# Kernel tuning notes

Hardware: AMD Instinct MI355X
Metric: run time of the kernel (lower is better)

## Reference

```python
import jax, jax.numpy as jnp
import numpy as np
from itertools import product

NUM_LEVELS = 4
NUM_FEATURES = 4
B, L = 32, 512

def build_kernel(num_features, num_levels):
    # signatory.all_words ordering: words grouped by length 1..num_levels, lexicographic within length
    words = [w for m in range(1, num_levels + 1) for w in product(range(num_features), repeat=m)]
    num_components = num_levels * (num_levels + 1) // 2
    k = np.zeros((num_components, num_features, len(words)), dtype=np.float32)
    for i, word in enumerate(words):
        m = len(word)
        start = m * (m - 1) // 2
        for j, axis in enumerate(word):
            k[start + j, axis, i] = 1.0
    return jnp.asarray(k)

def setup_inputs() -> dict:
    key = jax.random.key(0)
    x = jax.random.normal(key, (B, L, NUM_FEATURES), dtype=jnp.float32)
    return {"x": x, "kernel": build_kernel(NUM_FEATURES, NUM_LEVELS)}

def reference(x, kernel):
    Bn, Ln, F = x.shape
    NF = kernel.shape[-1]  # num_functionals = 340
    # path increments
    seq = x[:, 1:, :] - x[:, :-1, :]                      # (B, L-1, F)
    # lift: (C, B, L-1, NF), C = num_levels*(num_levels+1)/2 = 10
    M = jnp.einsum('blf,cfk->cblk', seq, kernel)
    # level-by-level recursion with independent weights, return_sequences=True
    # then summed over the stacked level axis (stack+sum == running sum of Y terms)
    sig = jnp.cumsum(M[0], axis=1)                        # level 1
    k = 1
    for m in range(1, NUM_LEVELS):
        R = M[k]; k += 1
        for _ in range(m):
            # tf.cumsum(..., exclusive=True) == inclusive cumsum minus self
            R = M[k] * (jnp.cumsum(R, axis=1) - R)
            k += 1
        sig = sig + jnp.cumsum(R, axis=1)
    # prepend zero time step -> (B, L, NF)
    sig = jnp.concatenate([jnp.zeros((Bn, 1, NF), dtype=x.dtype), sig], axis=1)
    # prepend constant-1 functional channel -> (B, L, NF+1)
    return jnp.concatenate([jnp.ones((Bn, Ln, 1), dtype=x.dtype), sig], axis=-1)
```

## Files before the change

### kernel.cpp

```cpp
#include <hip/hip_runtime.h>


#define SIG_B 32
#define SIG_L 512
#define SIG_NSTEP 511
#define SIG_ROW 341
#define SIG_CS 32
#define SIG_C 16
#define SIG_PAD 344

__global__ __launch_bounds__(256) void sigA(const float* __restrict__ x,
                                            float* __restrict__ Lsig) {
    const int bc = blockIdx.x;
    const int b = bc / SIG_C, c = bc % SIG_C;
    const int tid = threadIdx.x;
    const int t0 = c * SIG_CS;
    const int nt = min(SIG_CS, SIG_NSTEP - t0);

    __shared__ float dlds[SIG_CS * 4];
    const float* xb = x + ((size_t)b * SIG_L + t0) * 4;
    if (tid < nt) {
        float4 x0 = *(const float4*)(xb + tid * 4);
        float4 x1 = *(const float4*)(xb + (tid + 1) * 4);
        *(float4*)(dlds + tid * 4) =
            make_float4(x1.x - x0.x, x1.y - x0.y, x1.z - x0.z, x1.w - x0.w);
    }
    __syncthreads();

    const int a = tid >> 6, bb = (tid >> 4) & 3, cc = (tid >> 2) & 3, ee = tid & 3;
    float s1 = 0.f, s2 = 0.f, s3 = 0.f, s4 = 0.f;
    const float* dp = dlds;
    for (int t = 0; t < nt; ++t) {
        const float da = dp[a], db = dp[bb], dc = dp[cc], de = dp[ee];
        dp += 4;
        s4 = fmaf(s3, de, s4);
        s3 = fmaf(s2, dc, s3);
        s2 = fmaf(s1, db, s2);
        s1 += da;
    }
    float* Lr = Lsig + (size_t)bc * SIG_PAD;
    if ((tid & 63) == 0) Lr[1 + a] = s1;
    if ((tid & 15) == 0) Lr[5 + (tid >> 4)] = s2;
    if ((tid & 3) == 0)  Lr[21 + (tid >> 2)] = s3;
    Lr[85 + tid] = s4;
}

__global__ __launch_bounds__(256) void sigC(const float* __restrict__ x,
                                            const float* __restrict__ Lsig,
                                            float* __restrict__ out) {
    const int bc = blockIdx.x;
    const int b = bc / SIG_C, c = bc % SIG_C;
    const int tid = threadIdx.x;
    const int t0 = c * SIG_CS;
    const int nt = min(SIG_CS, SIG_NSTEP - t0);

    __shared__ float dlds[SIG_CS * 4];
    __shared__ float L[SIG_C * SIG_PAD];

    const float* xb = x + ((size_t)b * SIG_L + t0) * 4;
    if (tid < nt) {
        float4 x0 = *(const float4*)(xb + tid * 4);
        float4 x1 = *(const float4*)(xb + (tid + 1) * 4);
        *(float4*)(dlds + tid * 4) =
            make_float4(x1.x - x0.x, x1.y - x0.y, x1.z - x0.z, x1.w - x0.w);
    }
    {
        const float4* Lb4 = (const float4*)(Lsig + (size_t)b * SIG_C * SIG_PAD);
        float4* L4 = (float4*)L;
        const int n4 = c * (SIG_PAD / 4);
        for (int i = tid; i < n4; i += 256) L4[i] = Lb4[i];
    }
    __syncthreads();

    const int a = tid >> 6, bb = (tid >> 4) & 3, cc = (tid >> 2) & 3, ee = tid & 3;

    float p1 = 0.f, p2 = 0.f, p3 = 0.f, p4 = 0.f;
    for (int j = 0; j < c; ++j) {
        const float* Lc = L + j * SIG_PAD;
        const float l1a = Lc[1 + a], l1b = Lc[1 + bb], l1c = Lc[1 + cc], l1e = Lc[1 + ee];
        const float l2ab = Lc[5 + 4 * a + bb], l2bc = Lc[5 + 4 * bb + cc],
                    l2ce = Lc[5 + 4 * cc + ee];
        const float l3abc = Lc[21 + 16 * a + 4 * bb + cc],
                    l3bce = Lc[21 + 16 * bb + 4 * cc + ee];
        const float l4 = Lc[85 + tid];
        p4 += p3 * l1e + p2 * l2ce + p1 * l3bce + l4;
        p3 += p2 * l1c + p1 * l2bc + l3abc;
        p2 += p1 * l1b + l2ab;
        p1 += l1a;
    }

    float s1 = 0.f, s2 = 0.f, s3 = 0.f, s4 = 0.f;
    float x1_ = 0.f, x2_ = 0.f, x3_ = 0.f;
    float v1 = 0.f, v2 = 0.f;
    float u1 = 0.f;

    float* row = out + ((size_t)b * SIG_L + (t0 + 1)) * SIG_ROW;

    if (c == 0) {
        float* r0 = out + (size_t)b * SIG_L * SIG_ROW;
        if (tid == 0)        __builtin_nontemporal_store(1.0f, r0 + 0);
        if ((tid & 63) == 0) __builtin_nontemporal_store(0.f, r0 + 1 + a);
        if ((tid & 15) == 0) __builtin_nontemporal_store(0.f, r0 + 5 + (tid >> 4));
        if ((tid & 3) == 0)  __builtin_nontemporal_store(0.f, r0 + 21 + (tid >> 2));
        __builtin_nontemporal_store(0.f, r0 + 85 + tid);
    }

    const float* dp = dlds;
    for (int t = 0; t < nt; ++t) {
        const float da = dp[a], db = dp[bb], dc = dp[cc], de = dp[ee];
        dp += 4;
        s4 = fmaf(s3, de, s4); s3 = fmaf(s2, dc, s3); s2 = fmaf(s1, db, s2); s1 += da;
        x3_ = fmaf(x2_, de, x3_); x2_ = fmaf(x1_, dc, x2_); x1_ += db;
        v2 = fmaf(v1, de, v2); v1 += dc;
        u1 += de;

        if (tid == 0)        __builtin_nontemporal_store(1.0f, row + 0);
        if ((tid & 63) == 0) __builtin_nontemporal_store(p1 + s1, row + 1 + a);
        if ((tid & 15) == 0) __builtin_nontemporal_store(p2 + p1 * x1_ + s2,
                                                         row + 5 + (tid >> 4));
        if ((tid & 3) == 0)  __builtin_nontemporal_store(p3 + p2 * v1 + p1 * x2_ + s3,
                                                         row + 21 + (tid >> 2));
        __builtin_nontemporal_store(p4 + p3 * u1 + p2 * v2 + p1 * x3_ + s4,
                                    row + 85 + tid);
        row += SIG_ROW;
    }
}

extern "C" void kernel_launch(void* const* d_in, const int* in_sizes, int n_in,
                              void* d_out, int out_size, void* d_ws, size_t ws_size,
                              hipStream_t stream) {
    const float* x = (const float*)d_in[0];
    float* out = (float*)d_out;
    float* Lsig = (float*)d_ws;

    sigA<<<SIG_B * SIG_C, 256, 0, stream>>>(x, Lsig);
    sigC<<<SIG_B * SIG_C, 256, 0, stream>>>(x, Lsig, out);
}
```

Baseline: 22.20 us.

## Halve chunk length, double chunk count, and fully unroll time loops

```diff
diff --git a/kernel.cpp b/kernel.cpp
--- a/kernel.cpp
+++ b/kernel.cpp
@@ -5,8 +5,8 @@
 #define SIG_L 512
 #define SIG_NSTEP 511
 #define SIG_ROW 341
-#define SIG_CS 32
-#define SIG_C 16
+#define SIG_CS 16
+#define SIG_C 32
 #define SIG_PAD 344
 
 __global__ __launch_bounds__(256) void sigA(const float* __restrict__ x,
@@ -19,20 +19,24 @@
 
     __shared__ float dlds[SIG_CS * 4];
     const float* xb = x + ((size_t)b * SIG_L + t0) * 4;
-    if (tid < nt) {
-        float4 x0 = *(const float4*)(xb + tid * 4);
-        float4 x1 = *(const float4*)(xb + (tid + 1) * 4);
-        *(float4*)(dlds + tid * 4) =
-            make_float4(x1.x - x0.x, x1.y - x0.y, x1.z - x0.z, x1.w - x0.w);
+    if (tid < SIG_CS) {
+        float4 d = make_float4(0.f, 0.f, 0.f, 0.f);
+        if (tid < nt) {
+            float4 x0 = *(const float4*)(xb + tid * 4);
+            float4 x1 = *(const float4*)(xb + (tid + 1) * 4);
+            d = make_float4(x1.x - x0.x, x1.y - x0.y, x1.z - x0.z, x1.w - x0.w);
+        }
+        *(float4*)(dlds + tid * 4) = d;
     }
     __syncthreads();
 
     const int a = tid >> 6, bb = (tid >> 4) & 3, cc = (tid >> 2) & 3, ee = tid & 3;
     float s1 = 0.f, s2 = 0.f, s3 = 0.f, s4 = 0.f;
-    const float* dp = dlds;
-    for (int t = 0; t < nt; ++t) {
+
+#pragma unroll
+    for (int t = 0; t < SIG_CS; ++t) {
+        const float* dp = dlds + t * 4;
         const float da = dp[a], db = dp[bb], dc = dp[cc], de = dp[ee];
-        dp += 4;
         s4 = fmaf(s3, de, s4);
         s3 = fmaf(s2, dc, s3);
         s2 = fmaf(s1, db, s2);
@@ -58,17 +62,20 @@
     __shared__ float L[SIG_C * SIG_PAD];
 
     const float* xb = x + ((size_t)b * SIG_L + t0) * 4;
-    if (tid < nt) {
-        float4 x0 = *(const float4*)(xb + tid * 4);
-        float4 x1 = *(const float4*)(xb + (tid + 1) * 4);
-        *(float4*)(dlds + tid * 4) =
-            make_float4(x1.x - x0.x, x1.y - x0.y, x1.z - x0.z, x1.w - x0.w);
+    if (tid < SIG_CS) {
+        float4 d = make_float4(0.f, 0.f, 0.f, 0.f);
+        if (tid < nt) {
+            float4 x0 = *(const float4*)(xb + tid * 4);
+            float4 x1 = *(const float4*)(xb + (tid + 1) * 4);
+            d = make_float4(x1.x - x0.x, x1.y - x0.y, x1.z - x0.z, x1.w - x0.w);
+        }
+        *(float4*)(dlds + tid * 4) = d;
     }
     {
         const float4* Lb4 = (const float4*)(Lsig + (size_t)b * SIG_C * SIG_PAD);
-        float4* L4 = (float4*)L;
+        float4* L4p = (float4*)L;
         const int n4 = c * (SIG_PAD / 4);
-        for (int i = tid; i < n4; i += 256) L4[i] = Lb4[i];
+        for (int i = tid; i < n4; i += 256) L4p[i] = Lb4[i];
     }
     __syncthreads();
 
@@ -105,24 +112,26 @@
         __builtin_nontemporal_store(0.f, r0 + 85 + tid);
     }
 
-    const float* dp = dlds;
-    for (int t = 0; t < nt; ++t) {
+#pragma unroll
+    for (int t = 0; t < SIG_CS; ++t) {
+        const float* dp = dlds + t * 4;
         const float da = dp[a], db = dp[bb], dc = dp[cc], de = dp[ee];
-        dp += 4;
         s4 = fmaf(s3, de, s4); s3 = fmaf(s2, dc, s3); s2 = fmaf(s1, db, s2); s1 += da;
         x3_ = fmaf(x2_, de, x3_); x2_ = fmaf(x1_, dc, x2_); x1_ += db;
         v2 = fmaf(v1, de, v2); v1 += dc;
         u1 += de;
 
-        if (tid == 0)        __builtin_nontemporal_store(1.0f, row + 0);
-        if ((tid & 63) == 0) __builtin_nontemporal_store(p1 + s1, row + 1 + a);
-        if ((tid & 15) == 0) __builtin_nontemporal_store(p2 + p1 * x1_ + s2,
-                                                         row + 5 + (tid >> 4));
-        if ((tid & 3) == 0)  __builtin_nontemporal_store(p3 + p2 * v1 + p1 * x2_ + s3,
-                                                         row + 21 + (tid >> 2));
-        __builtin_nontemporal_store(p4 + p3 * u1 + p2 * v2 + p1 * x3_ + s4,
-                                    row + 85 + tid);
-        row += SIG_ROW;
+        if (t < nt) {
+            float* r = row + (size_t)t * SIG_ROW;
+            if (tid == 0)        __builtin_nontemporal_store(1.0f, r + 0);
+            if ((tid & 63) == 0) __builtin_nontemporal_store(p1 + s1, r + 1 + a);
+            if ((tid & 15) == 0) __builtin_nontemporal_store(p2 + p1 * x1_ + s2,
+                                                             r + 5 + (tid >> 4));
+            if ((tid & 3) == 0)  __builtin_nontemporal_store(p3 + p2 * v1 + p1 * x2_ + s3,
+                                                             r + 21 + (tid >> 2));
+            __builtin_nontemporal_store(p4 + p3 * u1 + p2 * v2 + p1 * x3_ + s4,
+                                        r + 85 + tid);
+        }
     }
 }
 
```

Result: slower. 29.21 us (+31.5%).
